# Kernel tuning notes

Hardware: AMD Instinct MI355X
Metric: run time of the kernel (lower is better)

The kernel has to match this reference:

```python
import jax, jax.numpy as jnp
import numpy as np

NLAT = 192  # octahedral O96-class grid


def _lons(nlat):
    half = [20 + 4 * i for i in range(nlat // 2)]
    return half + half[::-1]


def _dft_matrix(nlat, mmax):
    # Truncated per-ring real-DFT basis (torch.fft.rfft convention, 'forward' 1/n norm).
    # Ring j has nlon_j points; frequencies beyond its Nyquist (m > nlon_j//2) are zero.
    lons = _lons(nlat)
    max_nlon = max(lons)
    D = np.zeros((nlat, max_nlon, mmax), dtype=np.complex64)
    for j, n in enumerate(lons):
        keep = min(mmax, n // 2 + 1)
        k = np.arange(n)[:, None]
        m = np.arange(keep)[None, :]
        D[j, :n, :keep] = np.exp(-2j * np.pi * k * m / n) / n
    return D


def _legendre_weights(nlat, lmax, mmax):
    # Orthonormalized associated Legendre P_l^m at Gaussian latitudes (north->south),
    # with Gaussian quadrature weights and the 2*pi longitude factor folded in.
    xg, wg = np.polynomial.legendre.leggauss(nlat)
    x = xg[::-1].copy()
    w = wg[::-1].copy()
    s = np.sqrt(1.0 - x * x)
    leg = np.zeros((lmax, mmax, nlat))
    pmm = np.full(nlat, 1.0 / np.sqrt(4.0 * np.pi))
    for m in range(mmax):
        if m > 0:
            pmm = -np.sqrt((2 * m + 1) / (2.0 * m)) * s * pmm
        if m < lmax:
            leg[m, m] = pmm
        if m + 1 < lmax:
            leg[m + 1, m] = np.sqrt(2 * m + 3.0) * x * pmm
        for l in range(m + 2, lmax):
            a = np.sqrt((4.0 * l * l - 1.0) / (l * l - m * m))
            bb = np.sqrt(((2.0 * l + 1.0) * (l - 1 + m) * (l - 1 - m)) / ((2.0 * l - 3.0) * (l * l - m * m)))
            leg[l, m] = a * x * leg[l - 1, m] - bb * leg[l - 2, m]
    leg = 2.0 * np.pi * leg * w[None, None, :]
    return leg.astype(np.float32)


def setup_inputs() -> dict:
    key = jax.random.key(0)
    nlat = NLAT
    lmax = mmax = nlat // 2
    n_points = sum(_lons(nlat))  # 40320 for nlat=192
    data = jax.random.normal(key, (4, 1, 1, n_points, 100), dtype=jnp.float32)
    dft = jnp.asarray(_dft_matrix(nlat, mmax))
    leg = jnp.asarray(_legendre_weights(nlat, lmax, mmax))
    return {"data": data, "dft": dft, "leg": leg}


def reference(data, dft, leg):
    b, t, e, p, v = data.shape
    nlat, max_nlon, mmax = dft.shape
    lmax = leg.shape[0]
    lons = _lons(nlat)
    # static scatter map: flattened ragged rings -> [nlat, max_nlon] padded layout
    flat_idx = np.concatenate([j * max_nlon + np.arange(n) for j, n in enumerate(lons)])
    x = jnp.transpose(data, (0, 1, 2, 4, 3)).reshape(-1, p)  # [(b t e v), p]
    B = x.shape[0]
    x_pad = jnp.zeros((B, nlat * max_nlon), x.dtype).at[:, flat_idx].set(x)
    x_pad = x_pad.reshape(B, nlat, max_nlon)
    # ragged per-ring truncated real DFT, then associated-Legendre contraction
    f_hat = jnp.einsum('bjn,jnm->bjm', x_pad, dft)        # [B, nlat, mmax] complex
    coeffs = jnp.einsum('bjm,lmj->blm', f_hat, leg)       # [B, lmax, mmax] complex
    coeffs = coeffs.reshape(b, t, e, v, lmax, mmax)
    return jnp.transpose(coeffs, (0, 1, 2, 4, 5, 3))      # [b, t, e, yF, xF, v]
```

## Files before the change

### kernel.cpp

```cpp
#include <hip/hip_runtime.h>

#define NLAT 192
#define NPTS 40320
#define MMAX 96
#define LMAX 96
#define NV   100
#define MAXN 400
#define NB   400

typedef __attribute__((ext_vector_type(8))) short short8v;
typedef __attribute__((ext_vector_type(4))) float f32x4;

#define FSTR 40

static __device__ __forceinline__ float bits2f(unsigned int b) {
    union { unsigned int i; float f; } v; v.i = b; return v.f;
}
static __device__ __forceinline__ unsigned int f2bf(float f) {
    union { float f; unsigned int i; } v; v.f = f;
    return (v.i + 0x7FFFu + ((v.i >> 16) & 1u)) >> 16;
}

static __device__ __forceinline__ int Ssum(int n) {
    int q = n >> 3, r = n & 7; return 4 * q * (q - 1) + q * r;
}
static __device__ __forceinline__ int atoffk(int j) {
    if (j < 96) return 32 * (Ssum(j + 12) - 4);
    return 32 * (672 + 676 - Ssum(204 - j));
}
static __device__ __forceinline__ int kpad_of(int j) {
    return 32 * ((j < 96 ? (j + 12) : (203 - j)) >> 3);
}

typedef const __attribute__((address_space(1))) void* gas_ptr;
typedef __attribute__((address_space(3))) void* las_ptr;
static __device__ __forceinline__ void gload_lds16(const void* g, void* l) {
    __builtin_amdgcn_global_load_lds((gas_ptr)g, (las_ptr)l, 16, 0, 0);
}

__global__ __launch_bounds__(256) void leg_conv_kernel(
    const float* __restrict__ leg,
    unsigned short* __restrict__ legh,
    unsigned short* __restrict__ legl)
{
    int idx = blockIdx.x * 256 + threadIdx.x;
    if (idx >= 96 * 96 * 192) return;
    int j = idx % 192;
    int lm = idx / 192;
    int m = lm % 96, l = lm / 96;
    float v = leg[idx];
    unsigned int h = f2bf(v);
    unsigned int lo = f2bf(v - bits2f(h << 16));
    size_t o = ((size_t)m * 96 + l) * 192 + j;
    legh[o] = (unsigned short)h;
    legl[o] = (unsigned short)lo;
}

__global__ __launch_bounds__(256) void dft_transpose_kernel(
    const unsigned int* __restrict__ dftw,
    unsigned short* __restrict__ At)
{
    const int j = blockIdx.x;
    const int kpad = kpad_of(j);
    const int k0 = blockIdx.y * 32;
    if (k0 >= kpad) return;
    const int n = j < 96 ? 20 + 4 * j : 400 - 4 * (j - 96);
    unsigned short* abase = At + (size_t)atoffk(j) * 192;
    const int tid = threadIdx.x;
#pragma unroll
    for (int s = 0; s < 3; ++s) {
        int slot = s * 256 + tid;
        int row = slot % 192;
        int ch  = slot / 192;
        int m = row < 96 ? row : row - 96;
        bool isIm = row >= 96;
        const unsigned int* dp = dftw + ((size_t)j * MAXN + k0 + ch * 8) * 96 + m;
        unsigned short o[8];
#pragma unroll
        for (int i = 0; i < 8; ++i) {
            int k = k0 + ch * 8 + i;
            unsigned int v = (k < n) ? dp[(size_t)i * 96] : 0u;
            o[i] = isIm ? (unsigned short)(v >> 16) : (unsigned short)(v & 0xFFFFu);
        }
        uint4 pk;
        pk.x = (unsigned int)o[0] | ((unsigned int)o[1] << 16);
        pk.y = (unsigned int)o[2] | ((unsigned int)o[3] << 16);
        pk.z = (unsigned int)o[4] | ((unsigned int)o[5] << 16);
        pk.w = (unsigned int)o[6] | ((unsigned int)o[7] << 16);
        *(uint4*)(abase + (size_t)row * kpad + k0 + ch * 8) = pk;
    }
}

__global__ __launch_bounds__(256, 4) void dft_mfma_kernel(
    const float* __restrict__ data,
    const unsigned short* __restrict__ At,
    unsigned short* __restrict__ fh_hi,
    unsigned short* __restrict__ fh_lo,
    int c0, int cn)
{
    __shared__ unsigned short A_lds[192 * 32];
    __shared__ unsigned short Xh_lds[64 * 32];
    __shared__ unsigned short Xl_lds[64 * 32];

    const int bt  = blockIdx.x;
    const int p   = blockIdx.y;
    const int tid = threadIdx.x;
    const int w   = tid >> 6;
    const int l   = tid & 63;
    const int lr  = l & 15;
    const int kg  = l >> 4;
    const int kgp = kg ^ ((lr >> 1) & 3);

    const int Bb = c0 + bt * 50;
    const int bb = Bb / NV;
    const int vb = Bb % NV;
    const float* dbase = data + (size_t)bb * NPTS * NV + vb;

    const int xc  = tid >> 2;
    const int xch = tid & 3;
    const int xpc = xch ^ ((xc >> 1) & 3);

    for (int rr = 0; rr < 2; ++rr) {
        int j, n, start;
        if (rr == 0) { j = p;      n = 20 + 4 * p;  start = 2 * p * p + 18 * p; }
        else         { j = 96 + p; n = 400 - 4 * p; start = 20160 + 402 * p - 2 * p * p; }
        const int kpad = kpad_of(j);
        const unsigned short* abase = At + (size_t)atoffk(j) * 192;

        f32x4 acc[3][4];
#pragma unroll
        for (int i = 0; i < 3; ++i)
#pragma unroll
            for (int nt = 0; nt < 4; ++nt) acc[i][nt] = (f32x4){0.f, 0.f, 0.f, 0.f};

        for (int k0 = 0; k0 < kpad; k0 += 32) {
            __syncthreads();

#pragma unroll
            for (int s = 0; s < 3; ++s) {
                int slot = s * 256 + tid;
                int row  = slot >> 2;
                int chL  = (slot & 3) ^ ((row >> 1) & 3);
                const unsigned short* g = abase + (size_t)row * kpad + k0 + chL * 8;
                gload_lds16(g, &A_lds[s * 2048 + w * 512]);
            }

            float xv[8];
            {
                const float* sp = dbase + (size_t)(start + k0 + xch * 8) * NV + xc;
#pragma unroll
                for (int i = 0; i < 8; ++i) {
                    int k = k0 + xch * 8 + i;
                    xv[i] = (xc < 50 && k < n) ? sp[(size_t)i * NV] : 0.f;
                }
            }
            unsigned int hi4[4], lo4[4];
#pragma unroll
            for (int t2 = 0; t2 < 4; ++t2) {
                unsigned int x0 = __float_as_uint(xv[2 * t2]);
                unsigned int x1 = __float_as_uint(xv[2 * t2 + 1]);
                hi4[t2] = __builtin_amdgcn_perm(x1, x0, 0x07060302u);
                float r0 = xv[2 * t2]     - bits2f(x0 & 0xFFFF0000u);
                float r1 = xv[2 * t2 + 1] - bits2f(x1 & 0xFFFF0000u);
                unsigned int pk;
                asm("v_cvt_pk_bf16_f32 %0, %1, %2" : "=v"(pk) : "v"(r0), "v"(r1));
                lo4[t2] = pk;
            }
            *(uint4*)&Xh_lds[xc * 32 + xpc * 8] = (uint4){hi4[0], hi4[1], hi4[2], hi4[3]};
            *(uint4*)&Xl_lds[xc * 32 + xpc * 8] = (uint4){lo4[0], lo4[1], lo4[2], lo4[3]};
            __syncthreads();

            short8v a0 = *(const short8v*)&A_lds[((3 * w + 0) * 16 + lr) * 32 + kgp * 8];
            short8v a1 = *(const short8v*)&A_lds[((3 * w + 1) * 16 + lr) * 32 + kgp * 8];
            short8v a2 = *(const short8v*)&A_lds[((3 * w + 2) * 16 + lr) * 32 + kgp * 8];
#pragma unroll
            for (int nt = 0; nt < 4; ++nt) {
                short8v bh = *(const short8v*)&Xh_lds[(nt * 16 + lr) * 32 + kgp * 8];
                short8v bl = *(const short8v*)&Xl_lds[(nt * 16 + lr) * 32 + kgp * 8];
                acc[0][nt] = __builtin_amdgcn_mfma_f32_16x16x32_bf16(a0, bh, acc[0][nt], 0, 0, 0);
                acc[1][nt] = __builtin_amdgcn_mfma_f32_16x16x32_bf16(a1, bh, acc[1][nt], 0, 0, 0);
                acc[2][nt] = __builtin_amdgcn_mfma_f32_16x16x32_bf16(a2, bh, acc[2][nt], 0, 0, 0);
                acc[0][nt] = __builtin_amdgcn_mfma_f32_16x16x32_bf16(a0, bl, acc[0][nt], 0, 0, 0);
                acc[1][nt] = __builtin_amdgcn_mfma_f32_16x16x32_bf16(a1, bl, acc[1][nt], 0, 0, 0);
                acc[2][nt] = __builtin_amdgcn_mfma_f32_16x16x32_bf16(a2, bl, acc[2][nt], 0, 0, 0);
            }
        }

#pragma unroll
        for (int i = 0; i < 3; ++i)
#pragma unroll
            for (int nt = 0; nt < 4; ++nt) {
                int c = nt * 16 + lr;
                if (c < 50) {
                    int Brel = bt * 50 + c;
                    int mm0 = (3 * w + i) * 16 + kg * 4;
                    unsigned short* oh = fh_hi + ((size_t)j * 192 + mm0) * cn + Brel;
                    unsigned short* ol = fh_lo + ((size_t)j * 192 + mm0) * cn + Brel;
#pragma unroll
                    for (int r = 0; r < 4; ++r) {
                        float v = acc[i][nt][r];
                        unsigned int h = f2bf(v);
                        unsigned int lo = f2bf(v - bits2f(h << 16));
                        oh[(size_t)r * cn] = (unsigned short)h;
                        ol[(size_t)r * cn] = (unsigned short)lo;
                    }
                }
            }
    }
}

__global__ __launch_bounds__(256) void leg_mfma_kernel(
    const unsigned short* __restrict__ legh,
    const unsigned short* __restrict__ legl,
    const unsigned short* __restrict__ fh_hi,
    const unsigned short* __restrict__ fh_lo,
    unsigned int* __restrict__ out,
    int c0, int cn)
{
    __shared__ unsigned short A_lds[2 * 96 * FSTR];
    __shared__ unsigned short F_lds[2 * 2 * 64 * FSTR];

    const int m   = blockIdx.x;
    const int bt  = blockIdx.y;
    const int tid = threadIdx.x;
    const int w   = tid >> 6;
    const int l   = tid & 63;
    const int lr  = l & 15;
    const int kg  = l >> 4;

    f32x4 acc[6][2];
#pragma unroll
    for (int lt = 0; lt < 6; ++lt)
#pragma unroll
        for (int pl = 0; pl < 2; ++pl) acc[lt][pl] = (f32x4){0.f, 0.f, 0.f, 0.f};

    const unsigned int* lh32 = (const unsigned int*)legh;
    const unsigned int* ll32 = (const unsigned int*)legl;

    for (int j0 = 0; j0 < NLAT; j0 += 32) {
        __syncthreads();

#pragma unroll
        for (int s = 0; s < 12; ++s) {
            const int hl = (s >= 6) ? 1 : 0;
            int rem = tid + 256 * s - 1536 * hl;
            int lrow = rem >> 4;
            int ku = rem & 15;
            const unsigned int* src = hl ? ll32 : lh32;
            unsigned int v = src[((size_t)m * 96 + lrow) * 96 + (j0 >> 1) + ku];
            ((unsigned int*)A_lds)[(size_t)hl * 96 * (FSTR / 2) + lrow * (FSTR / 2) + ku] = v;
        }

#pragma unroll
        for (int s = 0; s < 13; ++s) {
            int q = tid + 256 * s;
            if (q < 3200) {
                int u  = q % 25;
                int r2 = q / 25;
                int jj = r2 & 31;
                int r3 = r2 >> 5;
                int pl = r3 & 1;
                int hl = r3 >> 1;
                const unsigned short* src = hl ? fh_lo : fh_hi;
                const unsigned int* s32 = (const unsigned int*)src;
                unsigned int v = s32[((size_t)(j0 + jj) * 192 + m + 96 * pl) * (cn >> 1)
                                     + bt * 25 + u];
                size_t base = ((size_t)(pl * 2 + hl) * 64 + 2 * u) * FSTR + jj;
                F_lds[base]        = (unsigned short)(v & 0xFFFFu);
                F_lds[base + FSTR] = (unsigned short)(v >> 16);
            }
        }
        __syncthreads();

        short8v fH[2], fL[2];
#pragma unroll
        for (int pl = 0; pl < 2; ++pl) {
            fH[pl] = *(const short8v*)&F_lds[((size_t)(pl * 2 + 0) * 64 + w * 16 + lr) * FSTR + kg * 8];
            fL[pl] = *(const short8v*)&F_lds[((size_t)(pl * 2 + 1) * 64 + w * 16 + lr) * FSTR + kg * 8];
        }
#pragma unroll
        for (int lt = 0; lt < 6; ++lt) {
            short8v ah = *(const short8v*)&A_lds[(size_t)(0 * 96 + lt * 16 + lr) * FSTR + kg * 8];
            short8v al = *(const short8v*)&A_lds[(size_t)(1 * 96 + lt * 16 + lr) * FSTR + kg * 8];
#pragma unroll
            for (int pl = 0; pl < 2; ++pl) {
                acc[lt][pl] = __builtin_amdgcn_mfma_f32_16x16x32_bf16(ah, fH[pl], acc[lt][pl], 0, 0, 0);
                acc[lt][pl] = __builtin_amdgcn_mfma_f32_16x16x32_bf16(ah, fL[pl], acc[lt][pl], 0, 0, 0);
                acc[lt][pl] = __builtin_amdgcn_mfma_f32_16x16x32_bf16(al, fH[pl], acc[lt][pl], 0, 0, 0);
            }
        }
    }

    int c = w * 16 + lr;
    if (c < 50) {
        int B = c0 + bt * 50 + c;
        int bb = B / NV, vv = B % NV;
#pragma unroll
        for (int lt = 0; lt < 6; ++lt) {
#pragma unroll
            for (int r = 0; r < 4; ++r) {
                int ll = lt * 16 + kg * 4 + r;
                out[(((size_t)bb * LMAX + ll) * MMAX + m) * NV + vv] =
                    f2bf(acc[lt][0][r]) | (f2bf(acc[lt][1][r]) << 16);
            }
        }
    }
}

extern "C" void kernel_launch(void* const* d_in, const int* in_sizes, int n_in,
                              void* d_out, int out_size, void* d_ws, size_t ws_size,
                              hipStream_t stream) {
    if (n_in != 3) return;

    const float* data = (const float*)d_in[0];
    const unsigned int* dftw = (const unsigned int*)d_in[1];
    const float* leg  = (const float*)d_in[2];
    unsigned int* out = (unsigned int*)d_out;

    const size_t LEGN = (size_t)96 * 96 * 192;
    const size_t LEGB = 2 * LEGN * sizeof(unsigned short);
    const size_t ATN  = (size_t)43008 * 192;
    const size_t ATB  = ATN * sizeof(unsigned short);
    const size_t rowb = (size_t)192 * 192 * 2 * sizeof(unsigned short);
    if (ws_size < LEGB + ATB + 50 * rowb) return;

    unsigned short* legh = (unsigned short*)d_ws;
    unsigned short* legl = legh + LEGN;
    unsigned short* At   = legl + LEGN;

    size_t maxrows = (ws_size - LEGB - ATB) / rowb;
    int chunk = (int)((maxrows / 50) * 50);
    if (chunk > NB) chunk = NB;

    leg_conv_kernel<<<dim3((96 * 96 * 192 + 255) / 256), dim3(256), 0, stream>>>(
        leg, legh, legl);
    dft_transpose_kernel<<<dim3(192, 13), dim3(256), 0, stream>>>(dftw, At);

    for (int c0 = 0; c0 < NB; c0 += chunk) {
        int cn = NB - c0 < chunk ? NB - c0 : chunk;
        unsigned short* fh_hi = At + ATN;
        unsigned short* fh_lo = fh_hi + (size_t)192 * 192 * cn;

        dim3 g1(cn / 50, 96);
        dft_mfma_kernel<<<g1, dim3(256), 0, stream>>>(data, At, fh_hi, fh_lo, c0, cn);
        dim3 g2(96, cn / 50);
        leg_mfma_kernel<<<g2, dim3(256), 0, stream>>>(legh, legl, fh_hi, fh_lo, out, c0, cn);
    }
}
```

Measured before the change: 105.3 us.

## Double-buffer DFT MFMA k-loop, tile A per k-step, one ring per block

The DFT matrix is stored tile-contiguously, with each 32-wide k-step as its own 192x32 block, so the per-step LDS loads are contiguous. The DFT kernel now double-buffers its A and X LDS tiles: it issues the next step's global loads before running the current step's MFMAs, which cuts one barrier per step. The grid is flattened so each block handles a single ring instead of a paired short and long ring. This doubles the block count and sizes each block's work to one ring, in exchange for double the LDS use and more registers held live across the MFMA section.

```diff
diff --git a/kernel.cpp b/kernel.cpp
--- a/kernel.cpp
+++ b/kernel.cpp
@@ -62,10 +62,11 @@
 {
     const int j = blockIdx.x;
     const int kpad = kpad_of(j);
-    const int k0 = blockIdx.y * 32;
+    const int t = blockIdx.y;
+    const int k0 = t * 32;
     if (k0 >= kpad) return;
     const int n = j < 96 ? 20 + 4 * j : 400 - 4 * (j - 96);
-    unsigned short* abase = At + (size_t)atoffk(j) * 192;
+    unsigned short* abase = At + (size_t)atoffk(j) * 192 + (size_t)t * 6144;
     const int tid = threadIdx.x;
 #pragma unroll
     for (int s = 0; s < 3; ++s) {
@@ -87,7 +88,7 @@
         pk.y = (unsigned int)o[2] | ((unsigned int)o[3] << 16);
         pk.z = (unsigned int)o[4] | ((unsigned int)o[5] << 16);
         pk.w = (unsigned int)o[6] | ((unsigned int)o[7] << 16);
-        *(uint4*)(abase + (size_t)row * kpad + k0 + ch * 8) = pk;
+        *(uint4*)(abase + (size_t)row * 32 + ch * 8) = pk;
     }
 }
 
@@ -98,12 +99,13 @@
     unsigned short* __restrict__ fh_lo,
     int c0, int cn)
 {
-    __shared__ unsigned short A_lds[192 * 32];
-    __shared__ unsigned short Xh_lds[64 * 32];
-    __shared__ unsigned short Xl_lds[64 * 32];
-
-    const int bt  = blockIdx.x;
-    const int p   = blockIdx.y;
+    __shared__ unsigned short A_lds[2][192 * 32];
+    __shared__ unsigned short Xh_lds[2][64 * 32];
+    __shared__ unsigned short Xl_lds[2][64 * 32];
+
+    const int id  = blockIdx.x;
+    const int j   = id % 192;
+    const int bt  = id / 192;
     const int tid = threadIdx.x;
     const int w   = tid >> 6;
     const int l   = tid & 63;
@@ -111,6 +113,12 @@
     const int kg  = l >> 4;
     const int kgp = kg ^ ((lr >> 1) & 3);
 
+    int n, start;
+    if (j < 96) { n = 20 + 4 * j; start = 2 * j * j + 18 * j; }
+    else { int jj = j - 96; n = 400 - 4 * jj; start = 20160 + 402 * jj - 2 * jj * jj; }
+    const int nsteps = kpad_of(j) >> 5;
+    const unsigned short* abase = At + (size_t)atoffk(j) * 192;
+
     const int Bb = c0 + bt * 50;
     const int bb = Bb / NV;
     const int vb = Bb % NV;
@@ -120,40 +128,83 @@
     const int xch = tid & 3;
     const int xpc = xch ^ ((xc >> 1) & 3);
 
-    for (int rr = 0; rr < 2; ++rr) {
-        int j, n, start;
-        if (rr == 0) { j = p;      n = 20 + 4 * p;  start = 2 * p * p + 18 * p; }
-        else         { j = 96 + p; n = 400 - 4 * p; start = 20160 + 402 * p - 2 * p * p; }
-        const int kpad = kpad_of(j);
-        const unsigned short* abase = At + (size_t)atoffk(j) * 192;
-
-        f32x4 acc[3][4];
-#pragma unroll
-        for (int i = 0; i < 3; ++i)
-#pragma unroll
-            for (int nt = 0; nt < 4; ++nt) acc[i][nt] = (f32x4){0.f, 0.f, 0.f, 0.f};
-
-        for (int k0 = 0; k0 < kpad; k0 += 32) {
-            __syncthreads();
-
+    f32x4 acc[3][4];
+#pragma unroll
+    for (int i = 0; i < 3; ++i)
+#pragma unroll
+        for (int nt = 0; nt < 4; ++nt) acc[i][nt] = (f32x4){0.f, 0.f, 0.f, 0.f};
+
+    float xv[8];
+
+    {
+        const float* sp = dbase + (size_t)(start + xch * 8) * NV + xc;
+#pragma unroll
+        for (int i = 0; i < 8; ++i) {
+            int k = xch * 8 + i;
+            xv[i] = (xc < 50 && k < n) ? sp[(size_t)i * NV] : 0.f;
+        }
+#pragma unroll
+        for (int s = 0; s < 3; ++s) {
+            int slot = s * 256 + tid;
+            int row  = slot >> 2;
+            int chs  = (slot & 3) ^ ((row >> 1) & 3);
+            gload_lds16(abase + (size_t)row * 32 + chs * 8, &A_lds[0][s * 2048 + w * 512]);
+        }
+        unsigned int hi4[4], lo4[4];
+#pragma unroll
+        for (int t2 = 0; t2 < 4; ++t2) {
+            unsigned int x0 = __float_as_uint(xv[2 * t2]);
+            unsigned int x1 = __float_as_uint(xv[2 * t2 + 1]);
+            hi4[t2] = __builtin_amdgcn_perm(x1, x0, 0x07060302u);
+            float r0 = xv[2 * t2]     - bits2f(x0 & 0xFFFF0000u);
+            float r1 = xv[2 * t2 + 1] - bits2f(x1 & 0xFFFF0000u);
+            unsigned int pk;
+            asm("v_cvt_pk_bf16_f32 %0, %1, %2" : "=v"(pk) : "v"(r0), "v"(r1));
+            lo4[t2] = pk;
+        }
+        *(uint4*)&Xh_lds[0][xc * 32 + xpc * 8] = (uint4){hi4[0], hi4[1], hi4[2], hi4[3]};
+        *(uint4*)&Xl_lds[0][xc * 32 + xpc * 8] = (uint4){lo4[0], lo4[1], lo4[2], lo4[3]};
+        __syncthreads();
+    }
+
+    int buf = 0;
+    for (int t = 0; t < nsteps; ++t) {
+        const int nb = buf ^ 1;
+        const bool pf = (t + 1 < nsteps);
+
+        if (pf) {
+            const float* sp = dbase + (size_t)(start + (t + 1) * 32 + xch * 8) * NV + xc;
+#pragma unroll
+            for (int i = 0; i < 8; ++i) {
+                int k = (t + 1) * 32 + xch * 8 + i;
+                xv[i] = (xc < 50 && k < n) ? sp[(size_t)i * NV] : 0.f;
+            }
 #pragma unroll
             for (int s = 0; s < 3; ++s) {
                 int slot = s * 256 + tid;
                 int row  = slot >> 2;
-                int chL  = (slot & 3) ^ ((row >> 1) & 3);
-                const unsigned short* g = abase + (size_t)row * kpad + k0 + chL * 8;
-                gload_lds16(g, &A_lds[s * 2048 + w * 512]);
-            }
-
-            float xv[8];
-            {
-                const float* sp = dbase + (size_t)(start + k0 + xch * 8) * NV + xc;
-#pragma unroll
-                for (int i = 0; i < 8; ++i) {
-                    int k = k0 + xch * 8 + i;
-                    xv[i] = (xc < 50 && k < n) ? sp[(size_t)i * NV] : 0.f;
-                }
-            }
+                int chs  = (slot & 3) ^ ((row >> 1) & 3);
+                gload_lds16(abase + (size_t)(t + 1) * 6144 + row * 32 + chs * 8,
+                            &A_lds[nb][s * 2048 + w * 512]);
+            }
+        }
+
+        short8v a0 = *(const short8v*)&A_lds[buf][((3 * w + 0) * 16 + lr) * 32 + kgp * 8];
+        short8v a1 = *(const short8v*)&A_lds[buf][((3 * w + 1) * 16 + lr) * 32 + kgp * 8];
+        short8v a2 = *(const short8v*)&A_lds[buf][((3 * w + 2) * 16 + lr) * 32 + kgp * 8];
+#pragma unroll
+        for (int nt = 0; nt < 4; ++nt) {
+            short8v bh = *(const short8v*)&Xh_lds[buf][(nt * 16 + lr) * 32 + kgp * 8];
+            short8v bl = *(const short8v*)&Xl_lds[buf][(nt * 16 + lr) * 32 + kgp * 8];
+            acc[0][nt] = __builtin_amdgcn_mfma_f32_16x16x32_bf16(a0, bh, acc[0][nt], 0, 0, 0);
+            acc[1][nt] = __builtin_amdgcn_mfma_f32_16x16x32_bf16(a1, bh, acc[1][nt], 0, 0, 0);
+            acc[2][nt] = __builtin_amdgcn_mfma_f32_16x16x32_bf16(a2, bh, acc[2][nt], 0, 0, 0);
+            acc[0][nt] = __builtin_amdgcn_mfma_f32_16x16x32_bf16(a0, bl, acc[0][nt], 0, 0, 0);
+            acc[1][nt] = __builtin_amdgcn_mfma_f32_16x16x32_bf16(a1, bl, acc[1][nt], 0, 0, 0);
+            acc[2][nt] = __builtin_amdgcn_mfma_f32_16x16x32_bf16(a2, bl, acc[2][nt], 0, 0, 0);
+        }
+
+        if (pf) {
             unsigned int hi4[4], lo4[4];
 #pragma unroll
             for (int t2 = 0; t2 < 4; ++t2) {
@@ -166,47 +217,33 @@
                 asm("v_cvt_pk_bf16_f32 %0, %1, %2" : "=v"(pk) : "v"(r0), "v"(r1));
                 lo4[t2] = pk;
             }
-            *(uint4*)&Xh_lds[xc * 32 + xpc * 8] = (uint4){hi4[0], hi4[1], hi4[2], hi4[3]};
-            *(uint4*)&Xl_lds[xc * 32 + xpc * 8] = (uint4){lo4[0], lo4[1], lo4[2], lo4[3]};
-            __syncthreads();
-
-            short8v a0 = *(const short8v*)&A_lds[((3 * w + 0) * 16 + lr) * 32 + kgp * 8];
-            short8v a1 = *(const short8v*)&A_lds[((3 * w + 1) * 16 + lr) * 32 + kgp * 8];
-            short8v a2 = *(const short8v*)&A_lds[((3 * w + 2) * 16 + lr) * 32 + kgp * 8];
-#pragma unroll
-            for (int nt = 0; nt < 4; ++nt) {
-                short8v bh = *(const short8v*)&Xh_lds[(nt * 16 + lr) * 32 + kgp * 8];
-                short8v bl = *(const short8v*)&Xl_lds[(nt * 16 + lr) * 32 + kgp * 8];
-                acc[0][nt] = __builtin_amdgcn_mfma_f32_16x16x32_bf16(a0, bh, acc[0][nt], 0, 0, 0);
-                acc[1][nt] = __builtin_amdgcn_mfma_f32_16x16x32_bf16(a1, bh, acc[1][nt], 0, 0, 0);
-                acc[2][nt] = __builtin_amdgcn_mfma_f32_16x16x32_bf16(a2, bh, acc[2][nt], 0, 0, 0);
-                acc[0][nt] = __builtin_amdgcn_mfma_f32_16x16x32_bf16(a0, bl, acc[0][nt], 0, 0, 0);
-                acc[1][nt] = __builtin_amdgcn_mfma_f32_16x16x32_bf16(a1, bl, acc[1][nt], 0, 0, 0);
-                acc[2][nt] = __builtin_amdgcn_mfma_f32_16x16x32_bf16(a2, bl, acc[2][nt], 0, 0, 0);
-            }
-        }
-
-#pragma unroll
-        for (int i = 0; i < 3; ++i)
-#pragma unroll
-            for (int nt = 0; nt < 4; ++nt) {
-                int c = nt * 16 + lr;
-                if (c < 50) {
-                    int Brel = bt * 50 + c;
-                    int mm0 = (3 * w + i) * 16 + kg * 4;
-                    unsigned short* oh = fh_hi + ((size_t)j * 192 + mm0) * cn + Brel;
-                    unsigned short* ol = fh_lo + ((size_t)j * 192 + mm0) * cn + Brel;
-#pragma unroll
-                    for (int r = 0; r < 4; ++r) {
-                        float v = acc[i][nt][r];
-                        unsigned int h = f2bf(v);
-                        unsigned int lo = f2bf(v - bits2f(h << 16));
-                        oh[(size_t)r * cn] = (unsigned short)h;
-                        ol[(size_t)r * cn] = (unsigned short)lo;
-                    }
+            *(uint4*)&Xh_lds[nb][xc * 32 + xpc * 8] = (uint4){hi4[0], hi4[1], hi4[2], hi4[3]};
+            *(uint4*)&Xl_lds[nb][xc * 32 + xpc * 8] = (uint4){lo4[0], lo4[1], lo4[2], lo4[3]};
+        }
+        __syncthreads();
+        buf = nb;
+    }
+
+#pragma unroll
+    for (int i = 0; i < 3; ++i)
+#pragma unroll
+        for (int nt = 0; nt < 4; ++nt) {
+            int c = nt * 16 + lr;
+            if (c < 50) {
+                int Brel = bt * 50 + c;
+                int mm0 = (3 * w + i) * 16 + kg * 4;
+                unsigned short* oh = fh_hi + ((size_t)j * 192 + mm0) * cn + Brel;
+                unsigned short* ol = fh_lo + ((size_t)j * 192 + mm0) * cn + Brel;
+#pragma unroll
+                for (int r = 0; r < 4; ++r) {
+                    float v = acc[i][nt][r];
+                    unsigned int h = f2bf(v);
+                    unsigned int lo = f2bf(v - bits2f(h << 16));
+                    oh[(size_t)r * cn] = (unsigned short)h;
+                    ol[(size_t)r * cn] = (unsigned short)lo;
                 }
             }
-    }
+        }
 }
 
 __global__ __launch_bounds__(256) void leg_mfma_kernel(
@@ -341,9 +378,10 @@
         unsigned short* fh_hi = At + ATN;
         unsigned short* fh_lo = fh_hi + (size_t)192 * 192 * cn;
 
-        dim3 g1(cn / 50, 96);
+        int nbt = cn / 50;
+        dim3 g1(192 * nbt);
         dft_mfma_kernel<<<g1, dim3(256), 0, stream>>>(data, At, fh_hi, fh_lo, c0, cn);
-        dim3 g2(96, cn / 50);
+        dim3 g2(96, nbt);
         leg_mfma_kernel<<<g2, dim3(256), 0, stream>>>(legh, legl, fh_hi, fh_lo, out, c0, cn);
     }
 }
```

Result: faster. 87.08 us (-17.3%).
